# Performance work log

Hardware: AMD Instinct MI355X
Metric: run time of the kernel (lower is better)

The kernel has to match this reference:

```python
import jax, jax.numpy as jnp
import numpy as np

N_NODES = 100000
N_EDGES = 1600000
D_FEAT = 128
CONV1_OUT = 64
CONV2_OUT = 32


def setup_inputs() -> dict:
    key = jax.random.key(0)
    k1, k2, k3, k4, k5, k6 = jax.random.split(key, 6)
    x = jax.random.normal(k1, (N_NODES, D_FEAT), dtype=jnp.float32)
    edge_row = jax.random.randint(k2, (N_EDGES,), 0, N_NODES, dtype=jnp.int32)
    edge_col = jax.random.randint(k3, (N_EDGES,), 0, N_NODES, dtype=jnp.int32)
    # normalized adjacency values (D^-1/2 A D^-1/2 entries are small positives)
    edge_val = jax.random.uniform(k4, (N_EDGES,), dtype=jnp.float32) / 16.0
    w1 = jax.random.normal(k5, (D_FEAT, CONV1_OUT), dtype=jnp.float32) / np.sqrt(D_FEAT)
    w2 = jax.random.normal(k6, (CONV1_OUT, CONV2_OUT), dtype=jnp.float32) / np.sqrt(CONV1_OUT)
    return {"x": x, "edge_row": edge_row, "edge_col": edge_col,
            "edge_val": edge_val, "w1": w1, "w2": w2}


def _spmm(edge_row, edge_col, edge_val, h):
    # out[i] = sum_{e: row[e]==i} val[e] * h[col[e]]  (sparse A @ h)
    gathered = edge_val[:, None] * h[edge_col]          # [E, F]
    return jax.ops.segment_sum(gathered, edge_row, num_segments=N_NODES)


def reference(x, edge_row, edge_col, edge_val, w1, w2):
    # Layer 1 (shared weights, relu); dropout inactive at inference.
    h = jnp.relu if False else None  # placeholder to keep linter quiet
    h1 = jax.nn.relu(_spmm(edge_row, edge_col, edge_val, x @ w1))   # [N, 64]
    # Layer 2 (per-cluster, identity activation)
    out = _spmm(edge_row, edge_col, edge_val, h1 @ w2)              # [N, 32]
    return out
```

## Files before the change

### kernel.cpp

```cpp
#include <hip/hip_runtime.h>

#define D_FEAT 128
#define C1 64
#define C2 32
#define BROWS 256
#define LOG_BROWS 8
#define BCAP  4608
#define NBMAX 512
#define GSTRIDE 16
#define CHUNK 2048
#define PTHREADS 512
#define EPT (CHUNK / PTHREADS)
#define WPAD 136
#define HPAD 72
#define VSCALE (32767.0f * 16.0f)
#define VDEQ (1.0f / VSCALE)

using bf16x8 = __attribute__((ext_vector_type(8))) __bf16;
using f32x4  = __attribute__((ext_vector_type(4))) float;

__device__ __forceinline__ unsigned short f2bf(float f) {
    unsigned u = __float_as_uint(f);
    u += 0x7fff + ((u >> 16) & 1);
    return (unsigned short)(u >> 16);
}
__device__ __forceinline__ float bflo(unsigned u) {
    return __uint_as_float(u << 16);
}
__device__ __forceinline__ float bfhi(unsigned u) {
    return __uint_as_float(u & 0xffff0000u);
}

__global__ __launch_bounds__(256) void zero_gcur(int* __restrict__ g, int count) {
    int i = blockIdx.x * 256 + threadIdx.x;
    if (i < count) g[i] = 0;
}

__global__ __launch_bounds__(256) void gemm1_mfma(const float* __restrict__ A,
                                                  const float* __restrict__ W,
                                                  unsigned short* __restrict__ C, int n) {
    __shared__ unsigned short wsb[C1][WPAD];
    __shared__ unsigned short xs[64][WPAD];

    const int t    = threadIdx.x;
    const int lane = t & 63;
    const int w    = t >> 6;
    const int row0 = blockIdx.x * 64;

    #pragma unroll
    for (int it = 0; it < 8; ++it) {
        const int nc = t & 63;
        const int k0 = ((t >> 6) + 4 * it) * 4;
        ushort4 o;
        o.x = f2bf(W[(k0 + 0) * C1 + nc]);
        o.y = f2bf(W[(k0 + 1) * C1 + nc]);
        o.z = f2bf(W[(k0 + 2) * C1 + nc]);
        o.w = f2bf(W[(k0 + 3) * C1 + nc]);
        *(ushort4*)&wsb[nc][k0] = o;
    }

    #pragma unroll
    for (int it = 0; it < 8; ++it) {
        const int qi = it * 256 + t;
        const int r  = qi >> 5;
        const int kq = (qi & 31) * 4;
        const int gr = row0 + r;
        float4 v = make_float4(0.f, 0.f, 0.f, 0.f);
        if (gr < n)
            v = *(const float4*)(A + (size_t)gr * D_FEAT + kq);
        ushort4 o;
        o.x = f2bf(v.x); o.y = f2bf(v.y); o.z = f2bf(v.z); o.w = f2bf(v.w);
        *(ushort4*)&xs[r][kq] = o;
    }
    __syncthreads();

    f32x4 acc[4];
    #pragma unroll
    for (int ct = 0; ct < 4; ++ct)
        acc[ct] = (f32x4){0.f, 0.f, 0.f, 0.f};

    const int mr = w * 16 + (lane & 15);
    const int kq = (lane >> 4) * 8;
    #pragma unroll
    for (int ks = 0; ks < 4; ++ks) {
        bf16x8 av = *(const bf16x8*)&xs[mr][ks * 32 + kq];
        #pragma unroll
        for (int ct = 0; ct < 4; ++ct) {
            bf16x8 bv = *(const bf16x8*)&wsb[ct * 16 + (lane & 15)][ks * 32 + kq];
            acc[ct] = __builtin_amdgcn_mfma_f32_16x16x32_bf16(av, bv, acc[ct], 0, 0, 0);
        }
    }

    const int rowbase = row0 + w * 16 + (lane >> 4) * 4;
    #pragma unroll
    for (int j = 0; j < 4; ++j) {
        const int gr = rowbase + j;
        if (gr < n) {
            #pragma unroll
            for (int ct = 0; ct < 4; ++ct)
                C[(size_t)gr * C1 + ct * 16 + (lane & 15)] = f2bf(acc[ct][j]);
        }
    }
}

__global__ __launch_bounds__(PTHREADS) void partition_kernel(const int* __restrict__ row,
                                                             const int* __restrict__ col,
                                                             const float* __restrict__ val,
                                                             int* __restrict__ gcur,
                                                             int2* __restrict__ bucket,
                                                             int E, int nb) {
    __shared__ int hist[NBMAX];
    __shared__ int base[NBMAX];
    __shared__ int cnt[NBMAX];
    const int t = threadIdx.x;
    const long long e0 = (long long)blockIdx.x * CHUNK;

    for (int i = t; i < nb; i += PTHREADS) {
        hist[i] = 0;
        cnt[i] = 0;
    }
    __syncthreads();

    int r[EPT];
    #pragma unroll
    for (int k = 0; k < EPT; k++) {
        long long i = e0 + k * PTHREADS + t;
        r[k] = (i < E) ? row[i] : -1;
        if (r[k] >= 0) atomicAdd(&hist[r[k] >> LOG_BROWS], 1);
    }
    __syncthreads();

    for (int i = t; i < nb; i += PTHREADS)
        if (hist[i] > 0)
            base[i] = atomicAdd(&gcur[i * GSTRIDE], hist[i]);
    __syncthreads();

    #pragma unroll
    for (int k = 0; k < EPT; k++) {
        long long i = e0 + k * PTHREADS + t;
        if (r[k] >= 0) {
            int b = r[k] >> LOG_BROWS;
            int off = base[b] + atomicAdd(&cnt[b], 1);
            if (off < BCAP)
                bucket[(size_t)b * BCAP + off] =
                    make_int2(((r[k] & (BROWS - 1)) << 17) | col[i], __float_as_int(val[i]));
        }
    }
}

__global__ __launch_bounds__(512) void bucket_scan(const int* __restrict__ gcur,
                                                   int* __restrict__ bstart, int nb) {
    __shared__ int s[512];
    const int t = threadIdx.x;
    int v = (t < nb) ? gcur[t * GSTRIDE] : 0;
    s[t] = v;
    __syncthreads();
    for (int off = 1; off < 512; off <<= 1) {
        int x = (t >= off) ? s[t - off] : 0;
        __syncthreads();
        s[t] += x;
        __syncthreads();
    }
    if (t < nb) bstart[t] = s[t] - v;
}

__global__ __launch_bounds__(256) void bucket_place(const int* __restrict__ gcur,
                                                    const int* __restrict__ bstart,
                                                    const int2* __restrict__ bucket,
                                                    int* __restrict__ ptr,
                                                    unsigned* __restrict__ csr, int n) {
    __shared__ int rhist[BROWS];
    __shared__ int rcur[BROWS];
    __shared__ int sscan[BROWS];
    __shared__ unsigned lbuf[BCAP];
    const int b = blockIdx.x;
    const int t = threadIdx.x;
    const int cnt = min(gcur[b * GSTRIDE], BCAP);
    const int gbase = bstart[b];
    const int2* bb = bucket + (size_t)b * BCAP;

    rhist[t] = 0;
    __syncthreads();

    for (int j = t; j < cnt; j += 256)
        atomicAdd(&rhist[bb[j].x >> 17], 1);
    __syncthreads();

    const int v = rhist[t];
    sscan[t] = v;
    __syncthreads();
    for (int off = 1; off < 256; off <<= 1) {
        int x = (t >= off) ? sscan[t - off] : 0;
        __syncthreads();
        sscan[t] += x;
        __syncthreads();
    }
    const int excl = sscan[t] - v;
    rcur[t] = excl;
    const int r0 = b * BROWS + t;
    if (r0 < n) ptr[r0] = gbase + excl;
    __syncthreads();

    for (int j = t; j < cnt; j += 256) {
        int2 w = bb[j];
        int lr = w.x >> 17;
        int pos = atomicAdd(&rcur[lr], 1);
        float fv = __int_as_float(w.y);
        unsigned vq = (unsigned)__float2int_rn(fv * VSCALE);
        vq = min(vq, 32767u);
        lbuf[pos] = ((unsigned)(w.x & 0x1FFFF) << 15) | vq;
    }
    __syncthreads();

    for (int j = t; j < cnt; j += 256)
        csr[(size_t)gbase + j] = lbuf[j];
}

__global__ __launch_bounds__(256) void spmm64_fused(const int* __restrict__ ptr,
                                                    const unsigned* __restrict__ csr,
                                                    const uint2* __restrict__ Hb,
                                                    const float* __restrict__ W2,
                                                    unsigned short* __restrict__ Zb,
                                                    int n, int E) {
    __shared__ unsigned short hlds[16][HPAD];
    __shared__ unsigned short w2t[C2][HPAD];

    const int t    = threadIdx.x;
    const int lane = t & 63;
    const int w    = t >> 6;
    const int g    = lane >> 4;
    const int lp   = lane & 15;
    const int rloc = w * 4 + g;
    const int row  = blockIdx.x * 16 + rloc;

    {
        const int nc = t & 31;
        const int k0 = (t >> 5) * 8;
        #pragma unroll
        for (int i = 0; i < 8; ++i)
            w2t[nc][k0 + i] = f2bf(W2[(k0 + i) * C2 + nc]);
    }

    int start = 0, end = 0;
    if (row < n) {
        start = ptr[row];
        end   = (row + 1 < n) ? ptr[row + 1] : E;
    }

    float4 A0 = make_float4(0.f, 0.f, 0.f, 0.f);
    float4 A1 = make_float4(0.f, 0.f, 0.f, 0.f);
    int e = start;
    for (; e + 7 < end; e += 8) {
        unsigned c[8];
        uint2 G[8];
        #pragma unroll
        for (int q = 0; q < 8; q++) c[q] = csr[e + q];
        #pragma unroll
        for (int q = 0; q < 8; q++) G[q] = Hb[(size_t)(c[q] >> 15) * 16 + lp];
        #pragma unroll
        for (int q = 0; q < 8; q++) {
            float v = (float)(c[q] & 0x7FFF) * VDEQ;
            if (q & 1) {
                A1.x += v * bflo(G[q].x); A1.y += v * bfhi(G[q].x);
                A1.z += v * bflo(G[q].y); A1.w += v * bfhi(G[q].y);
            } else {
                A0.x += v * bflo(G[q].x); A0.y += v * bfhi(G[q].x);
                A0.z += v * bflo(G[q].y); A0.w += v * bfhi(G[q].y);
            }
        }
    }
    if (e + 3 < end) {
        unsigned c[4];
        uint2 G[4];
        #pragma unroll
        for (int q = 0; q < 4; q++) c[q] = csr[e + q];
        #pragma unroll
        for (int q = 0; q < 4; q++) G[q] = Hb[(size_t)(c[q] >> 15) * 16 + lp];
        #pragma unroll
        for (int q = 0; q < 4; q++) {
            float v = (float)(c[q] & 0x7FFF) * VDEQ;
            if (q & 1) {
                A1.x += v * bflo(G[q].x); A1.y += v * bfhi(G[q].x);
                A1.z += v * bflo(G[q].y); A1.w += v * bfhi(G[q].y);
            } else {
                A0.x += v * bflo(G[q].x); A0.y += v * bfhi(G[q].x);
                A0.z += v * bflo(G[q].y); A0.w += v * bfhi(G[q].y);
            }
        }
        e += 4;
    }
    for (; e < end; e++) {
        unsigned c = csr[e];
        uint2 gg = Hb[(size_t)(c >> 15) * 16 + lp];
        float v = (float)(c & 0x7FFF) * VDEQ;
        A0.x += v * bflo(gg.x); A0.y += v * bfhi(gg.x);
        A0.z += v * bflo(gg.y); A0.w += v * bfhi(gg.y);
    }

    {
        ushort4 o;
        o.x = f2bf(fmaxf(A0.x + A1.x, 0.f));
        o.y = f2bf(fmaxf(A0.y + A1.y, 0.f));
        o.z = f2bf(fmaxf(A0.z + A1.z, 0.f));
        o.w = f2bf(fmaxf(A0.w + A1.w, 0.f));
        *(ushort4*)&hlds[rloc][lp * 4] = o;
    }
    __syncthreads();

    if (w == 0) {
        f32x4 acc[2];
        acc[0] = (f32x4){0.f, 0.f, 0.f, 0.f};
        acc[1] = (f32x4){0.f, 0.f, 0.f, 0.f};
        const int kq = (lane >> 4) * 8;
        #pragma unroll
        for (int ks = 0; ks < 2; ++ks) {
            bf16x8 av = *(const bf16x8*)&hlds[lane & 15][ks * 32 + kq];
            #pragma unroll
            for (int ct = 0; ct < 2; ++ct) {
                bf16x8 bv = *(const bf16x8*)&w2t[ct * 16 + (lane & 15)][ks * 32 + kq];
                acc[ct] = __builtin_amdgcn_mfma_f32_16x16x32_bf16(av, bv, acc[ct], 0, 0, 0);
            }
        }
        #pragma unroll
        for (int j = 0; j < 4; ++j) {
            const int grow = blockIdx.x * 16 + (lane >> 4) * 4 + j;
            if (grow < n) {
                #pragma unroll
                for (int ct = 0; ct < 2; ++ct)
                    Zb[(size_t)grow * C2 + ct * 16 + (lane & 15)] = f2bf(acc[ct][j]);
            }
        }
    }
}

__global__ __launch_bounds__(256) void spmm_csr32(const int* __restrict__ ptr,
                                                  const unsigned* __restrict__ csr,
                                                  const unsigned int* __restrict__ Zb,
                                                  float* __restrict__ OUT, int n, int E) {
    const int tid  = blockIdx.x * 256 + threadIdx.x;
    const int gwid = tid >> 6;
    const int lane = threadIdx.x & 63;
    const int g    = lane >> 4;
    const int lp   = lane & 15;
    const int row  = gwid * 4 + g;

    int start = 0, end = 0;
    if (row < n) {
        start = ptr[row];
        end   = (row + 1 < n) ? ptr[row + 1] : E;
    }

    float a0 = 0.f, a1 = 0.f, b0 = 0.f, b1 = 0.f;
    int e = start;
    for (; e + 7 < end; e += 8) {
        unsigned c[8];
        unsigned G[8];
        #pragma unroll
        for (int q = 0; q < 8; q++) c[q] = csr[e + q];
        #pragma unroll
        for (int q = 0; q < 8; q++) G[q] = Zb[(size_t)(c[q] >> 15) * 16 + lp];
        #pragma unroll
        for (int q = 0; q < 8; q++) {
            float v = (float)(c[q] & 0x7FFF) * VDEQ;
            if (q & 1) { b0 += v * bflo(G[q]); b1 += v * bfhi(G[q]); }
            else       { a0 += v * bflo(G[q]); a1 += v * bfhi(G[q]); }
        }
    }
    if (e + 3 < end) {
        unsigned c[4];
        unsigned G[4];
        #pragma unroll
        for (int q = 0; q < 4; q++) c[q] = csr[e + q];
        #pragma unroll
        for (int q = 0; q < 4; q++) G[q] = Zb[(size_t)(c[q] >> 15) * 16 + lp];
        #pragma unroll
        for (int q = 0; q < 4; q++) {
            float v = (float)(c[q] & 0x7FFF) * VDEQ;
            if (q & 1) { b0 += v * bflo(G[q]); b1 += v * bfhi(G[q]); }
            else       { a0 += v * bflo(G[q]); a1 += v * bfhi(G[q]); }
        }
        e += 4;
    }
    for (; e < end; e++) {
        unsigned c = csr[e];
        unsigned gg = Zb[(size_t)(c >> 15) * 16 + lp];
        float v = (float)(c & 0x7FFF) * VDEQ;
        a0 += v * bflo(gg); a1 += v * bfhi(gg);
    }
    if (row < n)
        *(float2*)(OUT + (size_t)row * C2 + 2 * lp) = make_float2(a0 + b0, a1 + b1);
}

extern "C" void kernel_launch(void* const* d_in, const int* in_sizes, int n_in,
                              void* d_out, int out_size, void* d_ws, size_t ws_size,
                              hipStream_t stream) {
    const float* x    = (const float*)d_in[0];
    const int*   erow = (const int*)d_in[1];
    const int*   ecol = (const int*)d_in[2];
    const float* eval = (const float*)d_in[3];
    const float* w1   = (const float*)d_in[4];
    const float* w2   = (const float*)d_in[5];
    float* out = (float*)d_out;

    const int n = in_sizes[0] / D_FEAT;
    const int E = in_sizes[1];

    const int nb = (n + BROWS - 1) / BROWS;
    const int pblocks = (E + CHUNK - 1) / CHUNK;

    unsigned short* y1b = (unsigned short*)d_ws;
    int2*  bucket = (int2*)(y1b + (size_t)n * C1);
    unsigned* csr = (unsigned*)(bucket + (size_t)nb * BCAP);
    int*   ptr    = (int*)(csr + E);
    int*   gcur   = ptr + n + 64;
    int*   bstart = gcur + NBMAX * GSTRIDE;
    unsigned short* zb = (unsigned short*)(bstart + NBMAX);

    {
        int count = nb * GSTRIDE;
        zero_gcur<<<(count + 255) / 256, 256, 0, stream>>>(gcur, count);
    }
    partition_kernel<<<pblocks, PTHREADS, 0, stream>>>(erow, ecol, eval, gcur, bucket, E, nb);
    bucket_scan<<<1, 512, 0, stream>>>(gcur, bstart, nb);
    bucket_place<<<nb, 256, 0, stream>>>(gcur, bstart, bucket, ptr, csr, n);

    gemm1_mfma<<<(n + 63) / 64, 256, 0, stream>>>(x, w1, y1b, n);

    spmm64_fused<<<(n + 15) / 16, 256, 0, stream>>>(ptr, csr, (const uint2*)y1b,
                                                    w2, zb, n, E);

    {
        int rows_per_block = 16;
        int blocks = (n + rows_per_block - 1) / rows_per_block;
        spmm_csr32<<<blocks, 256, 0, stream>>>(ptr, csr, (const unsigned int*)zb,
                                               out, n, E);
    }
}
```

Measured before the change: 125.6 us.

## Widen SpMM gathers to 16-byte loads with 8 lanes per row

Both SpMM kernels now give each row 8 lanes instead of 16. Each lane gathers wider vectors (uint4 for the 64-wide layer, uint2 for the 32-wide layer), so every wave covers twice as many rows and issues fewer, larger memory transactions. CSR index loads become nontemporal, and the fused kernel now runs two MFMA waves over 32 rows per block. The partition CHUNK grows to 8192, giving fewer partition blocks. In exchange, each lane does more work per edge, carries more registers and has less memory-level parallelism per row.

Result: faster. 120.6 us (-4.0%).

```diff
diff --git a/kernel.cpp b/kernel.cpp
--- a/kernel.cpp
+++ b/kernel.cpp
@@ -8,7 +8,7 @@
 #define BCAP  4608
 #define NBMAX 512
 #define GSTRIDE 16
-#define CHUNK 2048
+#define CHUNK 8192
 #define PTHREADS 512
 #define EPT (CHUNK / PTHREADS)
 #define WPAD 136
@@ -218,20 +218,20 @@
 
 __global__ __launch_bounds__(256) void spmm64_fused(const int* __restrict__ ptr,
                                                     const unsigned* __restrict__ csr,
-                                                    const uint2* __restrict__ Hb,
+                                                    const uint4* __restrict__ Hb,
                                                     const float* __restrict__ W2,
                                                     unsigned short* __restrict__ Zb,
                                                     int n, int E) {
-    __shared__ unsigned short hlds[16][HPAD];
+    __shared__ unsigned short hlds[32][HPAD];
     __shared__ unsigned short w2t[C2][HPAD];
 
     const int t    = threadIdx.x;
     const int lane = t & 63;
     const int w    = t >> 6;
-    const int g    = lane >> 4;
-    const int lp   = lane & 15;
-    const int rloc = w * 4 + g;
-    const int row  = blockIdx.x * 16 + rloc;
+    const int g    = lane >> 3;
+    const int lp   = lane & 7;
+    const int rloc = w * 8 + g;
+    const int row  = blockIdx.x * 32 + rloc;
 
     {
         const int nc = t & 31;
@@ -247,74 +247,71 @@
         end   = (row + 1 < n) ? ptr[row + 1] : E;
     }
 
-    float4 A0 = make_float4(0.f, 0.f, 0.f, 0.f);
-    float4 A1 = make_float4(0.f, 0.f, 0.f, 0.f);
+    float A0 = 0.f, A1 = 0.f, A2 = 0.f, A3 = 0.f;
+    float A4 = 0.f, A5 = 0.f, A6 = 0.f, A7 = 0.f;
     int e = start;
     for (; e + 7 < end; e += 8) {
         unsigned c[8];
-        uint2 G[8];
-        #pragma unroll
-        for (int q = 0; q < 8; q++) c[q] = csr[e + q];
-        #pragma unroll
-        for (int q = 0; q < 8; q++) G[q] = Hb[(size_t)(c[q] >> 15) * 16 + lp];
+        uint4 G[8];
+        #pragma unroll
+        for (int q = 0; q < 8; q++) c[q] = __builtin_nontemporal_load(&csr[e + q]);
+        #pragma unroll
+        for (int q = 0; q < 8; q++) G[q] = Hb[(size_t)(c[q] >> 15) * 8 + lp];
         #pragma unroll
         for (int q = 0; q < 8; q++) {
             float v = (float)(c[q] & 0x7FFF) * VDEQ;
-            if (q & 1) {
-                A1.x += v * bflo(G[q].x); A1.y += v * bfhi(G[q].x);
-                A1.z += v * bflo(G[q].y); A1.w += v * bfhi(G[q].y);
-            } else {
-                A0.x += v * bflo(G[q].x); A0.y += v * bfhi(G[q].x);
-                A0.z += v * bflo(G[q].y); A0.w += v * bfhi(G[q].y);
-            }
+            A0 += v * bflo(G[q].x); A1 += v * bfhi(G[q].x);
+            A2 += v * bflo(G[q].y); A3 += v * bfhi(G[q].y);
+            A4 += v * bflo(G[q].z); A5 += v * bfhi(G[q].z);
+            A6 += v * bflo(G[q].w); A7 += v * bfhi(G[q].w);
         }
     }
     if (e + 3 < end) {
         unsigned c[4];
-        uint2 G[4];
-        #pragma unroll
-        for (int q = 0; q < 4; q++) c[q] = csr[e + q];
-        #pragma unroll
-        for (int q = 0; q < 4; q++) G[q] = Hb[(size_t)(c[q] >> 15) * 16 + lp];
+        uint4 G[4];
+        #pragma unroll
+        for (int q = 0; q < 4; q++) c[q] = __builtin_nontemporal_load(&csr[e + q]);
+        #pragma unroll
+        for (int q = 0; q < 4; q++) G[q] = Hb[(size_t)(c[q] >> 15) * 8 + lp];
         #pragma unroll
         for (int q = 0; q < 4; q++) {
             float v = (float)(c[q] & 0x7FFF) * VDEQ;
-            if (q & 1) {
-                A1.x += v * bflo(G[q].x); A1.y += v * bfhi(G[q].x);
-                A1.z += v * bflo(G[q].y); A1.w += v * bfhi(G[q].y);
-            } else {
-                A0.x += v * bflo(G[q].x); A0.y += v * bfhi(G[q].x);
-                A0.z += v * bflo(G[q].y); A0.w += v * bfhi(G[q].y);
-            }
+            A0 += v * bflo(G[q].x); A1 += v * bfhi(G[q].x);
+            A2 += v * bflo(G[q].y); A3 += v * bfhi(G[q].y);
+            A4 += v * bflo(G[q].z); A5 += v * bfhi(G[q].z);
+            A6 += v * bflo(G[q].w); A7 += v * bfhi(G[q].w);
         }
         e += 4;
     }
     for (; e < end; e++) {
-        unsigned c = csr[e];
-        uint2 gg = Hb[(size_t)(c >> 15) * 16 + lp];
+        unsigned c = __builtin_nontemporal_load(&csr[e]);
+        uint4 gg = Hb[(size_t)(c >> 15) * 8 + lp];
         float v = (float)(c & 0x7FFF) * VDEQ;
-        A0.x += v * bflo(gg.x); A0.y += v * bfhi(gg.x);
-        A0.z += v * bflo(gg.y); A0.w += v * bfhi(gg.y);
+        A0 += v * bflo(gg.x); A1 += v * bfhi(gg.x);
+        A2 += v * bflo(gg.y); A3 += v * bfhi(gg.y);
+        A4 += v * bflo(gg.z); A5 += v * bfhi(gg.z);
+        A6 += v * bflo(gg.w); A7 += v * bfhi(gg.w);
     }
 
     {
-        ushort4 o;
-        o.x = f2bf(fmaxf(A0.x + A1.x, 0.f));
-        o.y = f2bf(fmaxf(A0.y + A1.y, 0.f));
-        o.z = f2bf(fmaxf(A0.z + A1.z, 0.f));
-        o.w = f2bf(fmaxf(A0.w + A1.w, 0.f));
-        *(ushort4*)&hlds[rloc][lp * 4] = o;
-    }
-    __syncthreads();
-
-    if (w == 0) {
+        ushort4 o0, o1;
+        o0.x = f2bf(fmaxf(A0, 0.f)); o0.y = f2bf(fmaxf(A1, 0.f));
+        o0.z = f2bf(fmaxf(A2, 0.f)); o0.w = f2bf(fmaxf(A3, 0.f));
+        o1.x = f2bf(fmaxf(A4, 0.f)); o1.y = f2bf(fmaxf(A5, 0.f));
+        o1.z = f2bf(fmaxf(A6, 0.f)); o1.w = f2bf(fmaxf(A7, 0.f));
+        *(ushort4*)&hlds[rloc][lp * 8]     = o0;
+        *(ushort4*)&hlds[rloc][lp * 8 + 4] = o1;
+    }
+    __syncthreads();
+
+    if (w < 2) {
         f32x4 acc[2];
         acc[0] = (f32x4){0.f, 0.f, 0.f, 0.f};
         acc[1] = (f32x4){0.f, 0.f, 0.f, 0.f};
         const int kq = (lane >> 4) * 8;
         #pragma unroll
         for (int ks = 0; ks < 2; ++ks) {
-            bf16x8 av = *(const bf16x8*)&hlds[lane & 15][ks * 32 + kq];
+            bf16x8 av = *(const bf16x8*)&hlds[w * 16 + (lane & 15)][ks * 32 + kq];
             #pragma unroll
             for (int ct = 0; ct < 2; ++ct) {
                 bf16x8 bv = *(const bf16x8*)&w2t[ct * 16 + (lane & 15)][ks * 32 + kq];
@@ -323,7 +320,7 @@
         }
         #pragma unroll
         for (int j = 0; j < 4; ++j) {
-            const int grow = blockIdx.x * 16 + (lane >> 4) * 4 + j;
+            const int grow = blockIdx.x * 32 + w * 16 + (lane >> 4) * 4 + j;
             if (grow < n) {
                 #pragma unroll
                 for (int ct = 0; ct < 2; ++ct)
@@ -335,14 +332,14 @@
 
 __global__ __launch_bounds__(256) void spmm_csr32(const int* __restrict__ ptr,
                                                   const unsigned* __restrict__ csr,
-                                                  const unsigned int* __restrict__ Zb,
+                                                  const uint2* __restrict__ Zb,
                                                   float* __restrict__ OUT, int n, int E) {
     const int tid  = blockIdx.x * 256 + threadIdx.x;
     const int gwid = tid >> 6;
     const int lane = threadIdx.x & 63;
-    const int g    = lane >> 4;
-    const int lp   = lane & 15;
-    const int row  = gwid * 4 + g;
+    const int g    = lane >> 3;
+    const int lp   = lane & 7;
+    const int row  = gwid * 8 + g;
 
     int start = 0, end = 0;
     if (row < n) {
@@ -350,45 +347,46 @@
         end   = (row + 1 < n) ? ptr[row + 1] : E;
     }
 
-    float a0 = 0.f, a1 = 0.f, b0 = 0.f, b1 = 0.f;
+    float a0 = 0.f, a1 = 0.f, a2 = 0.f, a3 = 0.f;
     int e = start;
     for (; e + 7 < end; e += 8) {
         unsigned c[8];
-        unsigned G[8];
-        #pragma unroll
-        for (int q = 0; q < 8; q++) c[q] = csr[e + q];
-        #pragma unroll
-        for (int q = 0; q < 8; q++) G[q] = Zb[(size_t)(c[q] >> 15) * 16 + lp];
+        uint2 G[8];
+        #pragma unroll
+        for (int q = 0; q < 8; q++) c[q] = __builtin_nontemporal_load(&csr[e + q]);
+        #pragma unroll
+        for (int q = 0; q < 8; q++) G[q] = Zb[(size_t)(c[q] >> 15) * 8 + lp];
         #pragma unroll
         for (int q = 0; q < 8; q++) {
             float v = (float)(c[q] & 0x7FFF) * VDEQ;
-            if (q & 1) { b0 += v * bflo(G[q]); b1 += v * bfhi(G[q]); }
-            else       { a0 += v * bflo(G[q]); a1 += v * bfhi(G[q]); }
+            a0 += v * bflo(G[q].x); a1 += v * bfhi(G[q].x);
+            a2 += v * bflo(G[q].y); a3 += v * bfhi(G[q].y);
         }
     }
     if (e + 3 < end) {
         unsigned c[4];
-        unsigned G[4];
-        #pragma unroll
-        for (int q = 0; q < 4; q++) c[q] = csr[e + q];
-        #pragma unroll
-        for (int q = 0; q < 4; q++) G[q] = Zb[(size_t)(c[q] >> 15) * 16 + lp];
+        uint2 G[4];
+        #pragma unroll
+        for (int q = 0; q < 4; q++) c[q] = __builtin_nontemporal_load(&csr[e + q]);
+        #pragma unroll
+        for (int q = 0; q < 4; q++) G[q] = Zb[(size_t)(c[q] >> 15) * 8 + lp];
         #pragma unroll
         for (int q = 0; q < 4; q++) {
             float v = (float)(c[q] & 0x7FFF) * VDEQ;
-            if (q & 1) { b0 += v * bflo(G[q]); b1 += v * bfhi(G[q]); }
-            else       { a0 += v * bflo(G[q]); a1 += v * bfhi(G[q]); }
+            a0 += v * bflo(G[q].x); a1 += v * bfhi(G[q].x);
+            a2 += v * bflo(G[q].y); a3 += v * bfhi(G[q].y);
         }
         e += 4;
     }
     for (; e < end; e++) {
-        unsigned c = csr[e];
-        unsigned gg = Zb[(size_t)(c >> 15) * 16 + lp];
+        unsigned c = __builtin_nontemporal_load(&csr[e]);
+        uint2 gg = Zb[(size_t)(c >> 15) * 8 + lp];
         float v = (float)(c & 0x7FFF) * VDEQ;
-        a0 += v * bflo(gg); a1 += v * bfhi(gg);
+        a0 += v * bflo(gg.x); a1 += v * bfhi(gg.x);
+        a2 += v * bflo(gg.y); a3 += v * bfhi(gg.y);
     }
     if (row < n)
-        *(float2*)(OUT + (size_t)row * C2 + 2 * lp) = make_float2(a0 + b0, a1 + b1);
+        *(float4*)(OUT + (size_t)row * C2 + 4 * lp) = make_float4(a0, a1, a2, a3);
 }
 
 extern "C" void kernel_launch(void* const* d_in, const int* in_sizes, int n_in,
@@ -426,13 +424,13 @@
 
     gemm1_mfma<<<(n + 63) / 64, 256, 0, stream>>>(x, w1, y1b, n);
 
-    spmm64_fused<<<(n + 15) / 16, 256, 0, stream>>>(ptr, csr, (const uint2*)y1b,
+    spmm64_fused<<<(n + 31) / 32, 256, 0, stream>>>(ptr, csr, (const uint4*)y1b,
                                                     w2, zb, n, E);
 
     {
-        int rows_per_block = 16;
+        int rows_per_block = 32;
         int blocks = (n + rows_per_block - 1) / rows_per_block;
-        spmm_csr32<<<blocks, 256, 0, stream>>>(ptr, csr, (const unsigned int*)zb,
+        spmm_csr32<<<blocks, 256, 0, stream>>>(ptr, csr, (const uint2*)zb,
                                                out, n, E);
     }
 }
```
